# Kernel tuning notes

Hardware: AMD Instinct MI355X
Metric: run time of the kernel (lower is better)

Reference implementation:

```python
import jax, jax.numpy as jnp
import numpy as np

N_NODES = 100000
N_EDGES = 1600000
BN_EPS = 1e-5
NUM_LAYER = 20


def setup_inputs() -> dict:
    key = jax.random.key(0)
    ks = jax.random.split(key, 10)
    inp = {
        "M": jax.random.normal(ks[0], (N_NODES, 3), dtype=jnp.float32),
        "H": jax.random.normal(ks[1], (N_EDGES, 3), dtype=jnp.float32),
        "edge_index": jax.random.randint(ks[2], (2, N_EDGES), 0, N_NODES, dtype=jnp.int32),
        # mlp_e: Linear(9,4) -> BN(4) -> ReLU -> Linear(4,3)
        "we_w1": jax.random.normal(ks[3], (9, 4), dtype=jnp.float32) * 0.3,
        "we_b1": jnp.zeros((4,), jnp.float32),
        "we_g1": jnp.ones((4,), jnp.float32),
        "we_be1": jnp.zeros((4,), jnp.float32),
        "we_w2": jax.random.normal(ks[4], (4, 3), dtype=jnp.float32) * 0.3,
        "we_b2": jnp.zeros((3,), jnp.float32),
        # mlp_v: Linear(6,3) -> BN(3) -> ReLU -> Linear(3,3)
        "wv_w1": jax.random.normal(ks[5], (6, 3), dtype=jnp.float32) * 0.3,
        "wv_b1": jnp.zeros((3,), jnp.float32),
        "wv_g1": jnp.ones((3,), jnp.float32),
        "wv_be1": jnp.zeros((3,), jnp.float32),
        "wv_w2": jax.random.normal(ks[6], (3, 3), dtype=jnp.float32) * 0.3,
        "wv_b2": jnp.zeros((3,), jnp.float32),
        # head: Linear(3,3) -> BN(3) -> ReLU -> Linear(3,2) -> Softmax
        "out_w1": jax.random.normal(ks[7], (3, 3), dtype=jnp.float32) * 0.3,
        "out_b1": jnp.zeros((3,), jnp.float32),
        "out_g": jnp.ones((3,), jnp.float32),
        "out_be": jnp.zeros((3,), jnp.float32),
        "out_w2": jax.random.normal(ks[8], (3, 2), dtype=jnp.float32) * 0.3,
        "out_b2": jnp.zeros((2,), jnp.float32),
    }
    return inp


def _bn(x, g, b):
    # BatchNorm1d in training mode: batch stats, biased variance
    m = jnp.mean(x, axis=0)
    v = jnp.mean(jnp.square(x - m), axis=0)
    return (x - m) * jax.lax.rsqrt(v + BN_EPS) * g + b


def reference(M, H, edge_index, we_w1, we_b1, we_g1, we_be1, we_w2, we_b2,
              wv_w1, wv_b1, wv_g1, wv_be1, wv_w2, wv_b2,
              out_w1, out_b1, out_g, out_be, out_w2, out_b2):
    src = edge_index[0]  # _j (source, flow=source_to_target)
    dst = edge_index[1]  # _i (target), also the aggregation index
    n = M.shape[0]

    def layer(carry, _):
        M, H = carry
        Mi = M[dst]  # [E,3] gather of target node feats
        Mj = M[src]  # [E,3] gather of source node feats
        e_in = jnp.concatenate([Mi, Mj, H], axis=1)  # [E,9]
        Hn = jax.nn.relu(_bn(e_in @ we_w1 + we_b1, we_g1, we_be1)) @ we_w2 + we_b2  # [E,3]
        v_in = jnp.concatenate([Mi, Hn], axis=1)  # [E,6]
        Mmsg = jax.nn.relu(_bn(v_in @ wv_w1 + wv_b1, wv_g1, wv_be1)) @ wv_w2 + wv_b2  # [E,3]
        Mn = jax.ops.segment_sum(Mmsg, dst, num_segments=n)  # scatter-add to targets
        return (Mn, Hn), None

    (M, H), _ = jax.lax.scan(layer, (M, H), None, length=NUM_LAYER)
    logits = jax.nn.relu(_bn(H @ out_w1 + out_b1, out_g, out_be)) @ out_w2 + out_b2  # [E,2]
    return jax.nn.softmax(logits, axis=1)
```

## Files before the change

### kernel.cpp

```cpp
#include <hip/hip_runtime.h>
#include <hip/hip_fp16.h>
#include <math.h>

#define NNODES 100000
#define NEDGES 1600000
#define NGROUP (NEDGES / 4)
#define NLAYERS 20
#define NB 256
#define BLK 256
#define GRIDE 1024
#define STRIDE (GRIDE * BLK)
#define GRIDL ((NGROUP + BLK - 1) / BLK)
#define NBLKN ((NNODES + 255) / 256)
#define GRIDN4 ((NNODES * 4 + BLK - 1) / BLK)

struct __align__(8) H4 { __half h[4]; };

template<int N>
__device__ __forceinline__ void block_stats_atomic(const float* vals, double* base) {
  __shared__ double sm[16][4];
  int lane = threadIdx.x & 63, wid = threadIdx.x >> 6;
  __syncthreads();
  #pragma unroll
  for (int n = 0; n < N; ++n) {
    double d = (double)vals[n];
    #pragma unroll
    for (int o = 32; o > 0; o >>= 1) d += __shfl_down(d, o, 64);
    if (lane == 0) sm[n][wid] = d;
  }
  __syncthreads();
  if (threadIdx.x < N) {
    double s = sm[threadIdx.x][0] + sm[threadIdx.x][1] + sm[threadIdx.x][2] + sm[threadIdx.x][3];
    atomicAdd(base + threadIdx.x, s);
  }
}

template<int NS>
__device__ __forceinline__ void bank_reduce(const double* __restrict__ acc, double* res) {
  __shared__ double part[4][8];
  int t = threadIdx.x;
  double v[NS];
  #pragma unroll
  for (int s = 0; s < NS; ++s) v[s] = acc[t * 8 + s];
  #pragma unroll
  for (int o = 32; o > 0; o >>= 1)
    #pragma unroll
    for (int s = 0; s < NS; ++s) v[s] += __shfl_down(v[s], o, 64);
  if ((t & 63) == 0) {
    int w = t >> 6;
    #pragma unroll
    for (int s = 0; s < NS; ++s) part[w][s] = v[s];
  }
  __syncthreads();
  #pragma unroll
  for (int s = 0; s < NS; ++s) res[s] = part[0][s] + part[1][s] + part[2][s] + part[3][s];
}

__device__ __forceinline__ void compute_x(const float4 mi, const float4 mj,
    float h0, float h1, float h2,
    const float* __restrict__ w, const float* __restrict__ b, float* x) {
  #pragma unroll
  for (int j = 0; j < 4; ++j) {
    float t = b[j];
    t += mi.x * w[0 * 4 + j]; t += mi.y * w[1 * 4 + j]; t += mi.z * w[2 * 4 + j];
    t += mj.x * w[3 * 4 + j]; t += mj.y * w[4 * 4 + j]; t += mj.z * w[5 * 4 + j];
    t += h0 * w[6 * 4 + j];  t += h1 * w[7 * 4 + j];  t += h2 * w[8 * 4 + j];
    x[j] = t;
  }
}

__global__ void __launch_bounds__(BLK) kz(const float* __restrict__ Min,
                                          float* __restrict__ M,
                                          int* __restrict__ hist,
                                          double* __restrict__ accs) {
  int tid = blockIdx.x * BLK + threadIdx.x;
  for (int v = tid; v < NNODES; v += STRIDE) {
    float4 m;
    m.x = Min[3 * v]; m.y = Min[3 * v + 1]; m.z = Min[3 * v + 2]; m.w = 0.f;
    *(float4*)(M + 4 * (size_t)v) = m;
    hist[v] = 0;
  }
  for (int i = tid; i < 3 * NB * 8; i += STRIDE) accs[i] = 0.0;
}

__global__ void __launch_bounds__(BLK) khr(const int* __restrict__ dst,
                                           int* __restrict__ hist,
                                           int* __restrict__ rankpos) {
  int g = blockIdx.x * BLK + threadIdx.x;
  if (g >= NGROUP) return;
  int4 d4 = ((const int4*)dst)[g];
  int4 r;
  r.x = atomicAdd(&hist[d4.x], 1);
  r.y = atomicAdd(&hist[d4.y], 1);
  r.z = atomicAdd(&hist[d4.z], 1);
  r.w = atomicAdd(&hist[d4.w], 1);
  ((int4*)rankpos)[g] = r;
}

__global__ void __launch_bounds__(256) ksA(const int* __restrict__ hist,
                                           int* __restrict__ bsum) {
  __shared__ int sm[256];
  int i = blockIdx.x * 256 + threadIdx.x;
  sm[threadIdx.x] = (i < NNODES) ? hist[i] : 0;
  __syncthreads();
  for (int o = 128; o > 0; o >>= 1) {
    if (threadIdx.x < o) sm[threadIdx.x] += sm[threadIdx.x + o];
    __syncthreads();
  }
  if (threadIdx.x == 0) bsum[blockIdx.x] = sm[0];
}

__global__ void __launch_bounds__(512) ksB(const int* __restrict__ bsum,
                                           int* __restrict__ bbase) {
  __shared__ int sm[512];
  int t = threadIdx.x;
  sm[t] = (t < NBLKN) ? bsum[t] : 0;
  __syncthreads();
  for (int o = 1; o < 512; o <<= 1) {
    int v = (t >= o) ? sm[t - o] : 0;
    __syncthreads();
    sm[t] += v;
    __syncthreads();
  }
  if (t < NBLKN) bbase[t] = (t == 0) ? 0 : sm[t - 1];
}

__global__ void __launch_bounds__(256) ksC(const int* __restrict__ hist,
                                           const int* __restrict__ bbase,
                                           int* __restrict__ off,
                                           int* __restrict__ dp) {
  __shared__ int sm[256];
  int t = threadIdx.x;
  int i = blockIdx.x * 256 + t;
  int v = (i < NNODES) ? hist[i] : 0;
  sm[t] = v;
  __syncthreads();
  for (int o = 1; o < 256; o <<= 1) {
    int u = (t >= o) ? sm[t - o] : 0;
    __syncthreads();
    sm[t] += u;
    __syncthreads();
  }
  if (i < NNODES) {
    int ex = bbase[blockIdx.x] + sm[t] - v;
    off[i] = ex;
    for (int e = ex; e < ex + v; ++e) dp[e] = i;
  }
  if (i == 0) off[NNODES] = NEDGES;
}

__global__ void __launch_bounds__(BLK) kpk(const int* __restrict__ dp,
                                           int2* __restrict__ dpp) {
  int g = blockIdx.x * BLK + threadIdx.x;
  if (g >= NGROUP) return;
  int4 d4 = ((const int4*)dp)[g];
  int2 o;
  o.x = d4.x;
  o.y = (d4.y - d4.x) | ((d4.z - d4.x) << 8) | ((d4.w - d4.x) << 16);
  dpp[g] = o;
}

__global__ void __launch_bounds__(BLK) kp1(const int* __restrict__ dst,
                                           const int* __restrict__ off,
                                           int* __restrict__ rankpos,
                                           int* __restrict__ eperm) {
  int g = blockIdx.x * BLK + threadIdx.x;
  if (g >= NGROUP) return;
  int4 d4 = ((const int4*)dst)[g];
  int4 r4 = ((int4*)rankpos)[g];
  int4 p4;
  p4.x = off[d4.x] + r4.x;
  p4.y = off[d4.y] + r4.y;
  p4.z = off[d4.z] + r4.z;
  p4.w = off[d4.w] + r4.w;
  int e = 4 * g;
  eperm[p4.x] = e; eperm[p4.y] = e + 1; eperm[p4.z] = e + 2; eperm[p4.w] = e + 3;
  ((int4*)rankpos)[g] = p4;
}

__global__ void __launch_bounds__(BLK) kp2(const int* __restrict__ src,
                                           const float* __restrict__ Hin,
                                           const int* __restrict__ eperm,
                                           int* __restrict__ sp,
                                           __half* __restrict__ Hp) {
  int g = blockIdx.x * BLK + threadIdx.x;
  if (g >= NGROUP) return;
  int4 e4 = ((const int4*)eperm)[g];
  int4 s4;
  s4.x = src[e4.x];
  s4.y = src[e4.y];
  s4.z = src[e4.z];
  s4.w = src[e4.w];
  __half hh[12];
  int ee[4] = {e4.x, e4.y, e4.z, e4.w};
  #pragma unroll
  for (int k = 0; k < 4; ++k) {
    size_t e3 = 3 * (size_t)ee[k];
    hh[3 * k]     = __float2half(Hin[e3]);
    hh[3 * k + 1] = __float2half(Hin[e3 + 1]);
    hh[3 * k + 2] = __float2half(Hin[e3 + 2]);
  }
  ((int4*)sp)[g] = s4;
  H4* Hv = (H4*)(Hp + 12 * (size_t)g);
  H4 a, b, c;
  #pragma unroll
  for (int i = 0; i < 4; ++i) { a.h[i] = hh[i]; b.h[i] = hh[4 + i]; c.h[i] = hh[8 + i]; }
  Hv[0] = a; Hv[1] = b; Hv[2] = c;
}

__global__ void __launch_bounds__(BLK) k1(
    const float* __restrict__ M, const __half* __restrict__ H,
    const int* __restrict__ sp, const int2* __restrict__ dpp,
    const float* __restrict__ W1, const float* __restrict__ b1,
    double* __restrict__ acc1, double* __restrict__ acc2) {
  int g = blockIdx.x * BLK + threadIdx.x;
  if (blockIdx.x == 0)
    for (int i = threadIdx.x; i < NB * 8; i += BLK) acc2[i] = 0.0;

  float sx[4] = {0, 0, 0, 0}, sq[4] = {0, 0, 0, 0};
  if (g < NGROUP) {
    int4 s4 = ((const int4*)sp)[g];
    int2 dppg = dpp[g];
    int d0 = dppg.x;
    int d1 = d0 + (dppg.y & 255);
    int d2 = d0 + ((dppg.y >> 8) & 255);
    int d3 = d0 + ((dppg.y >> 16) & 255);
    const H4* Hv = (const H4*)(H + 12 * (size_t)g);
    H4 a = Hv[0], b = Hv[1], c = Hv[2];
    float hf[12];
    #pragma unroll
    for (int i = 0; i < 4; ++i) {
      hf[i] = __half2float(a.h[i]); hf[4 + i] = __half2float(b.h[i]); hf[8 + i] = __half2float(c.h[i]);
    }
    float4 mi0 = *(const float4*)(M + 4 * (size_t)d0);
    float4 mj0 = *(const float4*)(M + 4 * (size_t)s4.x);
    float4 mi1 = *(const float4*)(M + 4 * (size_t)d1);
    float4 mj1 = *(const float4*)(M + 4 * (size_t)s4.y);
    float4 mi2 = *(const float4*)(M + 4 * (size_t)d2);
    float4 mj2 = *(const float4*)(M + 4 * (size_t)s4.z);
    float4 mi3 = *(const float4*)(M + 4 * (size_t)d3);
    float4 mj3 = *(const float4*)(M + 4 * (size_t)s4.w);
    float x[4][4];
    compute_x(mi0, mj0, hf[0], hf[1], hf[2],  W1, b1, x[0]);
    compute_x(mi1, mj1, hf[3], hf[4], hf[5],  W1, b1, x[1]);
    compute_x(mi2, mj2, hf[6], hf[7], hf[8],  W1, b1, x[2]);
    compute_x(mi3, mj3, hf[9], hf[10], hf[11], W1, b1, x[3]);
    #pragma unroll
    for (int k = 0; k < 4; ++k)
      #pragma unroll
      for (int j = 0; j < 4; ++j) { sx[j] += x[k][j]; sq[j] += x[k][j] * x[k][j]; }
  }
  float vals[8] = {sx[0], sx[1], sx[2], sx[3], sq[0], sq[1], sq[2], sq[3]};
  block_stats_atomic<8>(vals, acc1 + (size_t)(blockIdx.x & (NB - 1)) * 8);
}

__global__ void __launch_bounds__(BLK) k2(
    const float* __restrict__ M, const __half* __restrict__ H, __half* __restrict__ Hn,
    const int* __restrict__ sp, const int2* __restrict__ dpp,
    const float* __restrict__ W1, const float* __restrict__ b1,
    const float* __restrict__ g1, const float* __restrict__ be1,
    const float* __restrict__ W2, const float* __restrict__ b2,
    const float* __restrict__ V1, const float* __restrict__ vb1,
    const double* __restrict__ acc1, double* __restrict__ acc2,
    int isFinal,
    const float* __restrict__ OW1, const float* __restrict__ ob1,
    double* __restrict__ accF) {
  double red[8];
  bank_reduce<8>(acc1, red);
  float s1[4], t1[4];
  {
    const double invE = 1.0 / (double)NEDGES;
    #pragma unroll
    for (int j = 0; j < 4; ++j) {
      double m = red[j] * invE;
      double var = red[4 + j] * invE - m * m;
      double sc = (double)g1[j] / sqrt(var + 1e-5);
      s1[j] = (float)sc;
      t1[j] = (float)((double)be1[j] - m * sc);
    }
  }
  float sz[3] = {0, 0, 0}, szz[3] = {0, 0, 0}, sf[3] = {0, 0, 0}, sff[3] = {0, 0, 0};
  int g = blockIdx.x * BLK + threadIdx.x;
  if (g < NGROUP) {
    int4 s4 = ((const int4*)sp)[g];
    int2 dppg = dpp[g];
    int dd[4];
    dd[0] = dppg.x;
    dd[1] = dd[0] + (dppg.y & 255);
    dd[2] = dd[0] + ((dppg.y >> 8) & 255);
    dd[3] = dd[0] + ((dppg.y >> 16) & 255);
    const H4* Hv = (const H4*)(H + 12 * (size_t)g);
    H4 ha = Hv[0], hb = Hv[1], hc = Hv[2];
    float hf[12];
    #pragma unroll
    for (int i = 0; i < 4; ++i) {
      hf[i] = __half2float(ha.h[i]); hf[4 + i] = __half2float(hb.h[i]); hf[8 + i] = __half2float(hc.h[i]);
    }
    float4 mi[4], mj[4];
    mi[0] = *(const float4*)(M + 4 * (size_t)dd[0]);
    mj[0] = *(const float4*)(M + 4 * (size_t)s4.x);
    mi[1] = *(const float4*)(M + 4 * (size_t)dd[1]);
    mj[1] = *(const float4*)(M + 4 * (size_t)s4.y);
    mi[2] = *(const float4*)(M + 4 * (size_t)dd[2]);
    mj[2] = *(const float4*)(M + 4 * (size_t)s4.z);
    mi[3] = *(const float4*)(M + 4 * (size_t)dd[3]);
    mj[3] = *(const float4*)(M + 4 * (size_t)s4.w);
    __half hh[12];
    float hnr[4][3];
    #pragma unroll
    for (int k = 0; k < 4; ++k) {
      float x[4], y[4];
      compute_x(mi[k], mj[k], hf[3 * k], hf[3 * k + 1], hf[3 * k + 2], W1, b1, x);
      #pragma unroll
      for (int j = 0; j < 4; ++j) y[j] = fmaxf(x[j] * s1[j] + t1[j], 0.f);
      #pragma unroll
      for (int c = 0; c < 3; ++c) {
        float v = b2[c] + y[0] * W2[0 * 3 + c] + y[1] * W2[1 * 3 + c]
                        + y[2] * W2[2 * 3 + c] + y[3] * W2[3 * 3 + c];
        __half hv = __float2half(v);
        hh[3 * k + c] = hv;
        hnr[k][c] = __half2float(hv);
      }
      #pragma unroll
      for (int c = 0; c < 3; ++c) {
        float z = vb1[c] + mi[k].x * V1[0 * 3 + c] + mi[k].y * V1[1 * 3 + c] + mi[k].z * V1[2 * 3 + c]
                         + hnr[k][0] * V1[3 * 3 + c] + hnr[k][1] * V1[4 * 3 + c] + hnr[k][2] * V1[5 * 3 + c];
        sz[c] += z; szz[c] += z * z;
      }
      if (isFinal) {
        #pragma unroll
        for (int c = 0; c < 3; ++c) {
          float f = ob1[c] + hnr[k][0] * OW1[0 * 3 + c] + hnr[k][1] * OW1[1 * 3 + c] + hnr[k][2] * OW1[2 * 3 + c];
          sf[c] += f; sff[c] += f * f;
        }
      }
    }
    H4* Hw = (H4*)(Hn + 12 * (size_t)g);
    H4 oA, oB, oC;
    #pragma unroll
    for (int i = 0; i < 4; ++i) { oA.h[i] = hh[i]; oB.h[i] = hh[4 + i]; oC.h[i] = hh[8 + i]; }
    Hw[0] = oA; Hw[1] = oB; Hw[2] = oC;
  }
  size_t bank = (size_t)(blockIdx.x & (NB - 1)) * 8;
  float v6[6] = {sz[0], sz[1], sz[2], szz[0], szz[1], szz[2]};
  block_stats_atomic<6>(v6, acc2 + bank);
  if (isFinal) {
    float v6b[6] = {sf[0], sf[1], sf[2], sff[0], sff[1], sff[2]};
    block_stats_atomic<6>(v6b, accF + bank);
  }
}

__global__ void __launch_bounds__(BLK) k3(
    const float* __restrict__ M, const __half* __restrict__ Hn,
    const int* __restrict__ off,
    const float* __restrict__ V1, const float* __restrict__ vb1,
    const float* __restrict__ vg1, const float* __restrict__ vbe1,
    const float* __restrict__ V2, const float* __restrict__ vb2,
    const double* __restrict__ acc2, double* __restrict__ acc1,
    float* __restrict__ Mnew) {
  double red[6];
  bank_reduce<6>(acc2, red);
  float s2[3], t2[3];
  {
    const double invE = 1.0 / (double)NEDGES;
    #pragma unroll
    for (int c = 0; c < 3; ++c) {
      double m = red[c] * invE;
      double var = red[3 + c] * invE - m * m;
      double sc = (double)vg1[c] / sqrt(var + 1e-5);
      s2[c] = (float)sc;
      t2[c] = (float)((double)vbe1[c] - m * sc);
    }
  }
  if (blockIdx.x == 0)
    for (int i = threadIdx.x; i < NB * 8; i += BLK) acc1[i] = 0.0;

  int idx = blockIdx.x * BLK + threadIdx.x;
  int v = idx >> 2, q = idx & 3;
  if (v >= NNODES) return;
  float4 mi = *(const float4*)(M + 4 * (size_t)v);
  int e0 = off[v], e1 = off[v + 1];
  float a0 = 0.f, a1 = 0.f, a2v = 0.f;
  for (int e = e0 + q; e < e1; e += 4) {
    size_t e3 = 3 * (size_t)e;
    float h0 = __half2float(Hn[e3]), h1 = __half2float(Hn[e3 + 1]), h2 = __half2float(Hn[e3 + 2]);
    float y[3];
    #pragma unroll
    for (int c = 0; c < 3; ++c) {
      float z = vb1[c] + mi.x * V1[0 * 3 + c] + mi.y * V1[1 * 3 + c] + mi.z * V1[2 * 3 + c]
                       + h0 * V1[3 * 3 + c] + h1 * V1[4 * 3 + c] + h2 * V1[5 * 3 + c];
      y[c] = fmaxf(z * s2[c] + t2[c], 0.f);
    }
    a0  += vb2[0] + y[0] * V2[0] + y[1] * V2[3] + y[2] * V2[6];
    a1  += vb2[1] + y[0] * V2[1] + y[1] * V2[4] + y[2] * V2[7];
    a2v += vb2[2] + y[0] * V2[2] + y[1] * V2[5] + y[2] * V2[8];
  }
  a0  += __shfl_down(a0, 2, 4);  a0  += __shfl_down(a0, 1, 4);
  a1  += __shfl_down(a1, 2, 4);  a1  += __shfl_down(a1, 1, 4);
  a2v += __shfl_down(a2v, 2, 4); a2v += __shfl_down(a2v, 1, 4);
  if (q == 0) {
    float4 o; o.x = a0; o.y = a1; o.z = a2v; o.w = 0.f;
    *(float4*)(Mnew + 4 * (size_t)v) = o;
  }
}

__global__ void __launch_bounds__(BLK) f2(
    const __half* __restrict__ H, const int* __restrict__ pos,
    const float* __restrict__ OW1, const float* __restrict__ ob1,
    const float* __restrict__ og, const float* __restrict__ obe,
    const float* __restrict__ OW2, const float* __restrict__ ob2,
    const double* __restrict__ accF, float* __restrict__ out) {
  double red[6];
  bank_reduce<6>(accF, red);
  float sF[3], tF[3];
  {
    const double invE = 1.0 / (double)NEDGES;
    #pragma unroll
    for (int c = 0; c < 3; ++c) {
      double m = red[c] * invE;
      double var = red[3 + c] * invE - m * m;
      double sc = (double)og[c] / sqrt(var + 1e-5);
      sF[c] = (float)sc;
      tF[c] = (float)((double)obe[c] - m * sc);
    }
  }
  int g = blockIdx.x * BLK + threadIdx.x;
  if (g >= NGROUP) return;
  int4 p4 = ((const int4*)pos)[g];
  int p[4] = {p4.x, p4.y, p4.z, p4.w};
  float2 o[4];
  #pragma unroll
  for (int k = 0; k < 4; ++k) {
    size_t p3 = 3 * (size_t)p[k];
    float h0 = __half2float(H[p3]), h1 = __half2float(H[p3 + 1]), h2 = __half2float(H[p3 + 2]);
    float y[3];
    #pragma unroll
    for (int c = 0; c < 3; ++c) {
      float f = ob1[c] + h0 * OW1[0 * 3 + c] + h1 * OW1[1 * 3 + c] + h2 * OW1[2 * 3 + c];
      y[c] = fmaxf(f * sF[c] + tF[c], 0.f);
    }
    float l0 = ob2[0] + y[0] * OW2[0] + y[1] * OW2[2] + y[2] * OW2[4];
    float l1 = ob2[1] + y[0] * OW2[1] + y[1] * OW2[3] + y[2] * OW2[5];
    float mx = fmaxf(l0, l1);
    float e0 = __expf(l0 - mx), e1 = __expf(l1 - mx);
    float inv = 1.f / (e0 + e1);
    o[k].x = e0 * inv; o[k].y = e1 * inv;
  }
  float4 oA, oB;
  oA.x = o[0].x; oA.y = o[0].y; oA.z = o[1].x; oA.w = o[1].y;
  oB.x = o[2].x; oB.y = o[2].y; oB.z = o[3].x; oB.w = o[3].y;
  ((float4*)out)[2 * (size_t)g] = oA;
  ((float4*)out)[2 * (size_t)g + 1] = oB;
}

extern "C" void kernel_launch(void* const* d_in, const int* in_sizes, int n_in,
                              void* d_out, int out_size, void* d_ws, size_t ws_size,
                              hipStream_t stream) {
  const float* M_in   = (const float*)d_in[0];
  const float* H_in   = (const float*)d_in[1];
  const int*   ei     = (const int*)d_in[2];
  const float* we_w1  = (const float*)d_in[3];
  const float* we_b1  = (const float*)d_in[4];
  const float* we_g1  = (const float*)d_in[5];
  const float* we_be1 = (const float*)d_in[6];
  const float* we_w2  = (const float*)d_in[7];
  const float* we_b2  = (const float*)d_in[8];
  const float* wv_w1  = (const float*)d_in[9];
  const float* wv_b1  = (const float*)d_in[10];
  const float* wv_g1  = (const float*)d_in[11];
  const float* wv_be1 = (const float*)d_in[12];
  const float* wv_w2  = (const float*)d_in[13];
  const float* wv_b2  = (const float*)d_in[14];
  const float* out_w1 = (const float*)d_in[15];
  const float* out_b1 = (const float*)d_in[16];
  const float* out_g  = (const float*)d_in[17];
  const float* out_be = (const float*)d_in[18];
  const float* out_w2 = (const float*)d_in[19];
  const float* out_b2 = (const float*)d_in[20];
  const int* src = ei;
  const int* dst = ei + NEDGES;

  float* ws = (float*)d_ws;
  float* MA  = ws;
  float* MB  = ws + 400000;
  __half* Hp0 = (__half*)(ws + 800000);
  __half* Hp1 = (__half*)(ws + 3200000);
  int* eperm  = (int*)Hp1;
  int* ib      = (int*)(ws + 5600000);
  int* sp      = ib;
  int* dp      = ib + 1600000;
  int* rankpos = ib + 3200000;
  int2* dpp    = (int2*)(ib + 4800000);
  int* hist    = ib + 5600000;
  int* off     = ib + 5700000;
  int* bsum    = ib + 5800001;
  int* bbase   = ib + 5800401;
  double* accs = (double*)(ws + 5600000 + 5800802);
  double* acc1 = accs;
  double* acc2 = accs + NB * 8;
  double* accF = accs + 2 * NB * 8;

  kz<<<GRIDE, BLK, 0, stream>>>(M_in, MA, hist, accs);
  khr<<<GRIDL, BLK, 0, stream>>>(dst, hist, rankpos);
  ksA<<<NBLKN, 256, 0, stream>>>(hist, bsum);
  ksB<<<1, 512, 0, stream>>>(bsum, bbase);
  ksC<<<NBLKN, 256, 0, stream>>>(hist, bbase, off, dp);
  kpk<<<GRIDL, BLK, 0, stream>>>(dp, dpp);
  kp1<<<GRIDL, BLK, 0, stream>>>(dst, off, rankpos, eperm);
  kp2<<<GRIDL, BLK, 0, stream>>>(src, H_in, eperm, sp, Hp0);

  for (int l = 0; l < NLAYERS; ++l) {
    const float* Mc = (l & 1) ? MB : MA;
    float*       Mn = (l & 1) ? MA : MB;
    const __half* Hc = (l & 1) ? Hp1 : Hp0;
    __half*       Hw = (l & 1) ? Hp0 : Hp1;
    k1<<<GRIDL, BLK, 0, stream>>>(Mc, Hc, sp, dpp, we_w1, we_b1, acc1, acc2);
    k2<<<GRIDL, BLK, 0, stream>>>(Mc, Hc, Hw, sp, dpp, we_w1, we_b1, we_g1, we_be1,
                                  we_w2, we_b2, wv_w1, wv_b1, acc1, acc2,
                                  (l == NLAYERS - 1) ? 1 : 0, out_w1, out_b1, accF);
    if (l < NLAYERS - 1)
      k3<<<GRIDN4, BLK, 0, stream>>>(
          Mc, Hw, off, wv_w1, wv_b1, wv_g1, wv_be1, wv_w2, wv_b2, acc2, acc1, Mn);
  }
  f2<<<GRIDL, BLK, 0, stream>>>(Hp0, rankpos, out_w1, out_b1, out_g, out_be,
                                out_w2, out_b2, accF, (float*)d_out);
}
```

Measured before the change: 1.179 ms.

## Cache pre-BN edge activations in fp16 to skip k2 recompute and gathers

k1 now writes its pre-BatchNorm edge activations as fp16 to a workspace buffer, and its statistics are computed from those rounded values. k2 reads that buffer instead of re-gathering source-node features and edge features and recomputing the first linear layer. The aim is to trade random gathers and repeated maths in k2 for a streaming 8-byte-per-edge write and read. The block-level statistic shuffles drop from double to float, and the M and H ping-pong buffers become single in-place buffers. The change adds fp16 rounding of the intermediate activations and relies on the in-place M update in k3 being race-free.

```diff
diff --git a/kernel.cpp b/kernel.cpp
--- a/kernel.cpp
+++ b/kernel.cpp
@@ -18,19 +18,20 @@
 
 template<int N>
 __device__ __forceinline__ void block_stats_atomic(const float* vals, double* base) {
-  __shared__ double sm[16][4];
+  __shared__ float sm[8][4];
   int lane = threadIdx.x & 63, wid = threadIdx.x >> 6;
   __syncthreads();
   #pragma unroll
   for (int n = 0; n < N; ++n) {
-    double d = (double)vals[n];
+    float d = vals[n];
     #pragma unroll
     for (int o = 32; o > 0; o >>= 1) d += __shfl_down(d, o, 64);
     if (lane == 0) sm[n][wid] = d;
   }
   __syncthreads();
   if (threadIdx.x < N) {
-    double s = sm[threadIdx.x][0] + sm[threadIdx.x][1] + sm[threadIdx.x][2] + sm[threadIdx.x][3];
+    double s = (double)sm[threadIdx.x][0] + (double)sm[threadIdx.x][1]
+             + (double)sm[threadIdx.x][2] + (double)sm[threadIdx.x][3];
     atomicAdd(base + threadIdx.x, s);
   }
 }
@@ -210,6 +211,7 @@
 
 __global__ void __launch_bounds__(BLK) k1(
     const float* __restrict__ M, const __half* __restrict__ H,
+    __half* __restrict__ xb,
     const int* __restrict__ sp, const int2* __restrict__ dpp,
     const float* __restrict__ W1, const float* __restrict__ b1,
     double* __restrict__ acc1, double* __restrict__ acc2) {
@@ -245,19 +247,27 @@
     compute_x(mi1, mj1, hf[3], hf[4], hf[5],  W1, b1, x[1]);
     compute_x(mi2, mj2, hf[6], hf[7], hf[8],  W1, b1, x[2]);
     compute_x(mi3, mj3, hf[9], hf[10], hf[11], W1, b1, x[3]);
-    #pragma unroll
-    for (int k = 0; k < 4; ++k)
+    H4* xv = (H4*)xb + 4 * (size_t)g;
+    #pragma unroll
+    for (int k = 0; k < 4; ++k) {
+      H4 xo;
       #pragma unroll
-      for (int j = 0; j < 4; ++j) { sx[j] += x[k][j]; sq[j] += x[k][j] * x[k][j]; }
+      for (int j = 0; j < 4; ++j) {
+        __half hx = __float2half(x[k][j]);
+        xo.h[j] = hx;
+        float xr = __half2float(hx);
+        sx[j] += xr; sq[j] += xr * xr;
+      }
+      xv[k] = xo;
+    }
   }
   float vals[8] = {sx[0], sx[1], sx[2], sx[3], sq[0], sq[1], sq[2], sq[3]};
   block_stats_atomic<8>(vals, acc1 + (size_t)(blockIdx.x & (NB - 1)) * 8);
 }
 
 __global__ void __launch_bounds__(BLK) k2(
-    const float* __restrict__ M, const __half* __restrict__ H, __half* __restrict__ Hn,
-    const int* __restrict__ sp, const int2* __restrict__ dpp,
-    const float* __restrict__ W1, const float* __restrict__ b1,
+    const float* __restrict__ M, __half* __restrict__ Hn,
+    const __half* __restrict__ xb, const int2* __restrict__ dpp,
     const float* __restrict__ g1, const float* __restrict__ be1,
     const float* __restrict__ W2, const float* __restrict__ b2,
     const float* __restrict__ V1, const float* __restrict__ vb1,
@@ -282,55 +292,45 @@
   float sz[3] = {0, 0, 0}, szz[3] = {0, 0, 0}, sf[3] = {0, 0, 0}, sff[3] = {0, 0, 0};
   int g = blockIdx.x * BLK + threadIdx.x;
   if (g < NGROUP) {
-    int4 s4 = ((const int4*)sp)[g];
     int2 dppg = dpp[g];
     int dd[4];
     dd[0] = dppg.x;
     dd[1] = dd[0] + (dppg.y & 255);
     dd[2] = dd[0] + ((dppg.y >> 8) & 255);
     dd[3] = dd[0] + ((dppg.y >> 16) & 255);
-    const H4* Hv = (const H4*)(H + 12 * (size_t)g);
-    H4 ha = Hv[0], hb = Hv[1], hc = Hv[2];
-    float hf[12];
-    #pragma unroll
-    for (int i = 0; i < 4; ++i) {
-      hf[i] = __half2float(ha.h[i]); hf[4 + i] = __half2float(hb.h[i]); hf[8 + i] = __half2float(hc.h[i]);
-    }
-    float4 mi[4], mj[4];
+    float4 mi[4];
     mi[0] = *(const float4*)(M + 4 * (size_t)dd[0]);
-    mj[0] = *(const float4*)(M + 4 * (size_t)s4.x);
     mi[1] = *(const float4*)(M + 4 * (size_t)dd[1]);
-    mj[1] = *(const float4*)(M + 4 * (size_t)s4.y);
     mi[2] = *(const float4*)(M + 4 * (size_t)dd[2]);
-    mj[2] = *(const float4*)(M + 4 * (size_t)s4.z);
     mi[3] = *(const float4*)(M + 4 * (size_t)dd[3]);
-    mj[3] = *(const float4*)(M + 4 * (size_t)s4.w);
+    const H4* xv = (const H4*)xb + 4 * (size_t)g;
     __half hh[12];
-    float hnr[4][3];
     #pragma unroll
     for (int k = 0; k < 4; ++k) {
-      float x[4], y[4];
-      compute_x(mi[k], mj[k], hf[3 * k], hf[3 * k + 1], hf[3 * k + 2], W1, b1, x);
+      H4 xh = xv[k];
+      float y[4];
       #pragma unroll
-      for (int j = 0; j < 4; ++j) y[j] = fmaxf(x[j] * s1[j] + t1[j], 0.f);
+      for (int j = 0; j < 4; ++j)
+        y[j] = fmaxf(__half2float(xh.h[j]) * s1[j] + t1[j], 0.f);
+      float hr[3];
       #pragma unroll
       for (int c = 0; c < 3; ++c) {
         float v = b2[c] + y[0] * W2[0 * 3 + c] + y[1] * W2[1 * 3 + c]
                         + y[2] * W2[2 * 3 + c] + y[3] * W2[3 * 3 + c];
         __half hv = __float2half(v);
         hh[3 * k + c] = hv;
-        hnr[k][c] = __half2float(hv);
+        hr[c] = __half2float(hv);
       }
       #pragma unroll
       for (int c = 0; c < 3; ++c) {
         float z = vb1[c] + mi[k].x * V1[0 * 3 + c] + mi[k].y * V1[1 * 3 + c] + mi[k].z * V1[2 * 3 + c]
-                         + hnr[k][0] * V1[3 * 3 + c] + hnr[k][1] * V1[4 * 3 + c] + hnr[k][2] * V1[5 * 3 + c];
+                         + hr[0] * V1[3 * 3 + c] + hr[1] * V1[4 * 3 + c] + hr[2] * V1[5 * 3 + c];
         sz[c] += z; szz[c] += z * z;
       }
       if (isFinal) {
         #pragma unroll
         for (int c = 0; c < 3; ++c) {
-          float f = ob1[c] + hnr[k][0] * OW1[0 * 3 + c] + hnr[k][1] * OW1[1 * 3 + c] + hnr[k][2] * OW1[2 * 3 + c];
+          float f = ob1[c] + hr[0] * OW1[0 * 3 + c] + hr[1] * OW1[1 * 3 + c] + hr[2] * OW1[2 * 3 + c];
           sf[c] += f; sff[c] += f * f;
         }
       }
@@ -351,13 +351,12 @@
 }
 
 __global__ void __launch_bounds__(BLK) k3(
-    const float* __restrict__ M, const __half* __restrict__ Hn,
+    float* __restrict__ M, const __half* __restrict__ Hn,
     const int* __restrict__ off,
     const float* __restrict__ V1, const float* __restrict__ vb1,
     const float* __restrict__ vg1, const float* __restrict__ vbe1,
     const float* __restrict__ V2, const float* __restrict__ vb2,
-    const double* __restrict__ acc2, double* __restrict__ acc1,
-    float* __restrict__ Mnew) {
+    const double* __restrict__ acc2, double* __restrict__ acc1) {
   double red[6];
   bank_reduce<6>(acc2, red);
   float s2[3], t2[3];
@@ -400,7 +399,7 @@
   a2v += __shfl_down(a2v, 2, 4); a2v += __shfl_down(a2v, 1, 4);
   if (q == 0) {
     float4 o; o.x = a0; o.y = a1; o.z = a2v; o.w = 0.f;
-    *(float4*)(Mnew + 4 * (size_t)v) = o;
+    *(float4*)(M + 4 * (size_t)v) = o;
   }
 }
 
@@ -481,12 +480,10 @@
   const int* dst = ei + NEDGES;
 
   float* ws = (float*)d_ws;
-  float* MA  = ws;
-  float* MB  = ws + 400000;
-  __half* Hp0 = (__half*)(ws + 800000);
-  __half* Hp1 = (__half*)(ws + 3200000);
-  int* eperm  = (int*)Hp1;
-  int* ib      = (int*)(ws + 5600000);
+  float* M    = ws;
+  __half* Hp  = (__half*)(ws + 400000);
+  __half* xb  = (__half*)(ws + 2800000);
+  int* ib      = (int*)(ws + 6000000);
   int* sp      = ib;
   int* dp      = ib + 1600000;
   int* rankpos = ib + 3200000;
@@ -495,33 +492,30 @@
   int* off     = ib + 5700000;
   int* bsum    = ib + 5800001;
   int* bbase   = ib + 5800401;
-  double* accs = (double*)(ws + 5600000 + 5800802);
+  double* accs = (double*)(ws + 6000000 + 5800802);
   double* acc1 = accs;
   double* acc2 = accs + NB * 8;
   double* accF = accs + 2 * NB * 8;
-
-  kz<<<GRIDE, BLK, 0, stream>>>(M_in, MA, hist, accs);
+  int* eperm   = dp;
+
+  kz<<<GRIDE, BLK, 0, stream>>>(M_in, M, hist, accs);
   khr<<<GRIDL, BLK, 0, stream>>>(dst, hist, rankpos);
   ksA<<<NBLKN, 256, 0, stream>>>(hist, bsum);
   ksB<<<1, 512, 0, stream>>>(bsum, bbase);
   ksC<<<NBLKN, 256, 0, stream>>>(hist, bbase, off, dp);
   kpk<<<GRIDL, BLK, 0, stream>>>(dp, dpp);
   kp1<<<GRIDL, BLK, 0, stream>>>(dst, off, rankpos, eperm);
-  kp2<<<GRIDL, BLK, 0, stream>>>(src, H_in, eperm, sp, Hp0);
+  kp2<<<GRIDL, BLK, 0, stream>>>(src, H_in, eperm, sp, Hp);
 
   for (int l = 0; l < NLAYERS; ++l) {
-    const float* Mc = (l & 1) ? MB : MA;
-    float*       Mn = (l & 1) ? MA : MB;
-    const __half* Hc = (l & 1) ? Hp1 : Hp0;
-    __half*       Hw = (l & 1) ? Hp0 : Hp1;
-    k1<<<GRIDL, BLK, 0, stream>>>(Mc, Hc, sp, dpp, we_w1, we_b1, acc1, acc2);
-    k2<<<GRIDL, BLK, 0, stream>>>(Mc, Hc, Hw, sp, dpp, we_w1, we_b1, we_g1, we_be1,
+    k1<<<GRIDL, BLK, 0, stream>>>(M, Hp, xb, sp, dpp, we_w1, we_b1, acc1, acc2);
+    k2<<<GRIDL, BLK, 0, stream>>>(M, Hp, xb, dpp, we_g1, we_be1,
                                   we_w2, we_b2, wv_w1, wv_b1, acc1, acc2,
                                   (l == NLAYERS - 1) ? 1 : 0, out_w1, out_b1, accF);
     if (l < NLAYERS - 1)
       k3<<<GRIDN4, BLK, 0, stream>>>(
-          Mc, Hw, off, wv_w1, wv_b1, wv_g1, wv_be1, wv_w2, wv_b2, acc2, acc1, Mn);
-  }
-  f2<<<GRIDL, BLK, 0, stream>>>(Hp0, rankpos, out_w1, out_b1, out_g, out_be,
+          M, Hp, off, wv_w1, wv_b1, wv_g1, wv_be1, wv_w2, wv_b2, acc2, acc1);
+  }
+  f2<<<GRIDL, BLK, 0, stream>>>(Hp, rankpos, out_w1, out_b1, out_g, out_be,
                                 out_w2, out_b2, accF, (float*)d_out);
 }
```

Result: faster. 1.151 ms (-2.4%).
